# Optimization experiments

Measured on AMD Instinct MI355X. Metric: run time of the kernel, lower is better.

Reference implementation:

```python
import jax, jax.numpy as jnp
import numpy as np

N_FIELDS = 8
HIDDEN = 128
GEO = 15
APP = 32
N_PTS = 524288


def setup_inputs() -> dict:
    key = jax.random.key(0)
    ks = jax.random.split(key, 12)
    cin = 3 + GEO + APP  # color-net input dim = 50
    s = 0.05
    return {
        "positions": jax.random.normal(ks[0], (N_PTS, 3), jnp.float32),
        "directions": jax.random.normal(ks[1], (N_PTS, 3), jnp.float32),
        "appearance_embedding": jax.random.normal(ks[2], (N_PTS, APP), jnp.float32),
        "centroids": jax.random.normal(ks[3], (N_FIELDS, 3), jnp.float32),
        "Wd1": jax.random.normal(ks[4], (N_FIELDS, 3, HIDDEN), jnp.float32) * s,
        "bd1": jnp.zeros((N_FIELDS, HIDDEN), jnp.float32),
        "Wd2": jax.random.normal(ks[5], (N_FIELDS, HIDDEN, 1 + GEO), jnp.float32) * s,
        "bd2": jnp.zeros((N_FIELDS, 1 + GEO), jnp.float32),
        "Wc1": jax.random.normal(ks[6], (N_FIELDS, cin, HIDDEN), jnp.float32) * s,
        "bc1": jnp.zeros((N_FIELDS, HIDDEN), jnp.float32),
        "Wc2": jax.random.normal(ks[7], (N_FIELDS, HIDDEN, 3), jnp.float32) * s,
        "bc2": jnp.zeros((N_FIELDS, 3), jnp.float32),
    }


def reference(positions, directions, appearance_embedding, centroids,
              Wd1, bd1, Wd2, bd2, Wc1, bc1, Wc2, bc2):
    # --- routing: nearest centroid (cdist + argmin); squared dist has same argmin ---
    d2 = jnp.sum((positions[:, None, :] - centroids[None, :, :]) ** 2, axis=-1)  # [N, F]
    assign = jnp.argmin(d2, axis=1)  # [N] int

    n = positions.shape[0]
    density = jnp.zeros((n, 1), positions.dtype)
    rgb = jnp.zeros((n, 3), positions.dtype)

    # dispatch/combine: masked dense evaluation per field (small fixed field count)
    for i in range(N_FIELDS):
        mask = (assign == i)[:, None]
        # field.density_fn: 2-layer MLP, trunc_exp density activation
        h = jax.nn.relu(positions @ Wd1[i] + bd1[i])          # [N, H]
        dout = h @ Wd2[i] + bd2[i]                            # [N, 1+GEO]
        dens_i = jnp.exp(dout[:, :1])                         # trunc_exp
        geo_i = dout[:, 1:]                                   # density embedding
        # field.get_outputs: color head on (dirs, geo_feat, appearance)
        cin = jnp.concatenate([directions, geo_i, appearance_embedding], axis=-1)
        hc = jax.nn.relu(cin @ Wc1[i] + bc1[i])               # [N, H]
        rgb_i = jax.nn.sigmoid(hc @ Wc2[i] + bc2[i])          # [N, 3]
        density = jnp.where(mask, dens_i, density)
        rgb = jnp.where(mask, rgb_i, rgb)

    # outputs concatenated: [density | rgb] -> [N, 4]
    return jnp.concatenate([density, rgb], axis=-1)
```

## Files before the change

kernel.cpp:

```cpp
#include <hip/hip_runtime.h>
#include <math.h>

#define NF 8
#define HID 128
#define TILE 576
#define NIT 9

typedef _Float16 f16;
typedef _Float16 h2 __attribute__((ext_vector_type(2)));
typedef _Float16 f16x8 __attribute__((ext_vector_type(8)));
typedef float f32x4 __attribute__((ext_vector_type(4)));
typedef unsigned int u32;
typedef u32 u32x2 __attribute__((ext_vector_type(2)));
typedef u32 u32x4 __attribute__((ext_vector_type(4)));

__device__ __forceinline__ u32 pk(float a, float b) {
    return __builtin_bit_cast(u32, __builtin_amdgcn_cvt_pkrtz(a, b));
}
__device__ __forceinline__ float dot2a(u32 a, u32 b, float c) {
    return __builtin_amdgcn_fdot2(__builtin_bit_cast(h2, a),
                                  __builtin_bit_cast(h2, b), c, false);
}


__device__ __forceinline__ int assign_field(float px, float py, float pz,
                                            const float* __restrict__ cen) {
    int best = 0;
    float bd = 3.4e38f;
#pragma unroll
    for (int k = 0; k < NF; ++k) {
        float dx = px - cen[k * 3 + 0];
        float dy = py - cen[k * 3 + 1];
        float dz = pz - cen[k * 3 + 2];
        float d = fmaf(dx, dx, fmaf(dy, dy, dz * dz));
        if (d < bd) { bd = d; best = k; }
    }
    return best;
}

__global__ void k_count(const float* __restrict__ pos, const float* __restrict__ cen,
                        int n, int* __restrict__ blockcnt) {
    __shared__ int lc[NF];
    int tid = threadIdx.x;
    if (tid < NF) lc[tid] = 0;
    __syncthreads();
    int i4 = blockIdx.x * blockDim.x + tid;
    int base = i4 * 4;
    if (base + 3 < n) {
        const float4* p4 = (const float4*)pos;
        float4 a = p4[i4 * 3 + 0];
        float4 b = p4[i4 * 3 + 1];
        float4 c = p4[i4 * 3 + 2];
        atomicAdd(&lc[assign_field(a.x, a.y, a.z, cen)], 1);
        atomicAdd(&lc[assign_field(a.w, b.x, b.y, cen)], 1);
        atomicAdd(&lc[assign_field(b.z, b.w, c.x, cen)], 1);
        atomicAdd(&lc[assign_field(c.y, c.z, c.w, cen)], 1);
    } else {
        for (int i = base; i < n; ++i)
            atomicAdd(&lc[assign_field(pos[3 * i], pos[3 * i + 1], pos[3 * i + 2], cen)], 1);
    }
    __syncthreads();
    if (tid < NF) blockcnt[blockIdx.x * NF + tid] = lc[tid];
}

__global__ void k_scatscan(const float* __restrict__ pos, const float* __restrict__ cen,
                           int n, int nb, int* __restrict__ ws) {
    const int tid = threadIdx.x;
    const int f = tid >> 6, lane = tid & 63;
    const int* c = ws + 32;
    int* perm = ws + 32 + nb * NF;
    __shared__ int totals[NF], pres[NF], starts[NF], cur[NF];

    int tot = 0, pre = 0;
    for (int b = lane; b < nb; b += 64) {
        int v = c[b * NF + f];
        tot += v;
        if (b < (int)blockIdx.x) pre += v;
    }
#pragma unroll
    for (int d = 1; d < 64; d <<= 1) {
        tot += __shfl_xor(tot, d, 64);
        pre += __shfl_xor(pre, d, 64);
    }
    if (lane == 0) { totals[f] = tot; pres[f] = pre; }
    __syncthreads();
    if (tid == 0) {
        int s = 0, tp = 0;
        for (int k = 0; k < NF; ++k) {
            starts[k] = s;
            if (blockIdx.x == 0) {
                ws[k] = totals[k];
                ws[8 + k] = s;
                ws[16 + k] = tp;
            }
            s += totals[k];
            tp += (totals[k] + TILE - 1) / TILE;
        }
        if (blockIdx.x == 0) ws[24] = tp;
    }
    __syncthreads();
    if (tid < NF) cur[tid] = starts[tid] + pres[tid];
    __syncthreads();

    int i4 = blockIdx.x * blockDim.x + tid;
    int base = i4 * 4;
    if (base + 3 < n) {
        const float4* p4 = (const float4*)pos;
        float4 a = p4[i4 * 3 + 0];
        float4 b = p4[i4 * 3 + 1];
        float4 cc = p4[i4 * 3 + 2];
        int f0 = assign_field(a.x, a.y, a.z, cen);
        int f1 = assign_field(a.w, b.x, b.y, cen);
        int f2 = assign_field(b.z, b.w, cc.x, cen);
        int f3 = assign_field(cc.y, cc.z, cc.w, cen);
        perm[atomicAdd(&cur[f0], 1)] = base;
        perm[atomicAdd(&cur[f1], 1)] = base + 1;
        perm[atomicAdd(&cur[f2], 1)] = base + 2;
        perm[atomicAdd(&cur[f3], 1)] = base + 3;
    } else {
        for (int i = base; i < n; ++i) {
            int ff = assign_field(pos[3 * i], pos[3 * i + 1], pos[3 * i + 2], cen);
            perm[atomicAdd(&cur[ff], 1)] = i;
        }
    }
}

__global__ __launch_bounds__(256, 3) void k_main(
    const float* __restrict__ positions, const float* __restrict__ directions,
    const float* __restrict__ app,
    const float* __restrict__ Wd1, const float* __restrict__ bd1,
    const float* __restrict__ Wd2, const float* __restrict__ bd2,
    const float* __restrict__ Wc1, const float* __restrict__ bc1,
    const float* __restrict__ Wc2, const float* __restrict__ bc2,
    const int* __restrict__ ws, int nb, float* __restrict__ out) {
    const int b = blockIdx.x;
    if (b >= ws[24]) return;
    int f = 0;
#pragma unroll
    for (int k = 1; k < NF; ++k) if (b >= ws[16 + k]) f = k;
    const int tile = b - ws[16 + f];
    const int cnt = ws[f];
    const int start = ws[8 + f];
    const int* perm = ws + 32 + nb * NF;
    const int tid = threadIdx.x;
    const int w = tid >> 6, lane = tid & 63;
    const int pt = lane & 15, quad = lane >> 4;

    __shared__ __align__(16) f16 sWc1t[HID * 72];
    __shared__ __align__(16) u32 sWc2p[64 * 4];
    __shared__ __align__(16) int sIdx[4][16];
    __shared__ __align__(16) u32x2 sDir[4][16];
    __shared__ __align__(16) f16 sGeo[4][16][16];
    __shared__ __align__(16) f16 sH[4][16 * 136];

    if (tid < HID) {
        int h = tid;
        f16* row = &sWc1t[h * 72];
        const float* Wf = Wc1 + f * 50 * HID;
        row[0] = (f16)Wf[0 * HID + h];
        row[1] = (f16)Wf[1 * HID + h];
        row[2] = (f16)Wf[2 * HID + h];
        row[3] = (f16)bc1[f * HID + h];
        row[4] = 0; row[5] = 0; row[6] = 0; row[7] = 0;
        for (int a = 0; a < 32; ++a) row[8 + a] = (f16)Wf[(18 + a) * HID + h];
        for (int g = 0; g < 15; ++g) row[40 + g] = (f16)Wf[(3 + g) * HID + h];
        for (int z = 55; z < 72; ++z) row[z] = 0;
    }
    if (tid >= 128 && tid < 192) {
        int hp = tid - 128;
        const float* W2 = Wc2 + f * HID * 3;
        sWc2p[hp * 4 + 0] = pk(W2[(2 * hp) * 3 + 0], W2[(2 * hp + 1) * 3 + 0]);
        sWc2p[hp * 4 + 1] = pk(W2[(2 * hp) * 3 + 1], W2[(2 * hp + 1) * 3 + 1]);
        sWc2p[hp * 4 + 2] = pk(W2[(2 * hp) * 3 + 2], W2[(2 * hp + 1) * 3 + 2]);
        sWc2p[hp * 4 + 3] = 0;
    }
    if (lane < 16) sGeo[w][pt][15] = (f16)0.f;

    u32 wd1a0[8], wd1a1[8];
    if (quad == 0) {
        const float* W1 = Wd1 + f * 3 * HID;
        const float* B1 = bd1 + f * HID;
#pragma unroll
        for (int mt = 0; mt < 8; ++mt) {
            int m = 16 * mt + pt;
            wd1a0[mt] = pk(W1[m], W1[HID + m]);
            wd1a1[mt] = pk(W1[2 * HID + m], B1[m]);
        }
    } else {
#pragma unroll
        for (int mt = 0; mt < 8; ++mt) { wd1a0[mt] = 0; wd1a1[mt] = 0; }
    }
    f16x8 wd2b[4];
    {
        const float* W2d = Wd2 + f * HID * 16;
#pragma unroll
        for (int s = 0; s < 4; ++s) {
            u32x4 v;
#pragma unroll
            for (int jp = 0; jp < 4; ++jp) {
                int k = quad * 8 + 32 * s + 2 * jp;
                v[jp] = pk(W2d[k * 16 + pt], W2d[(k + 1) * 16 + pt]);
            }
            wd2b[s] = __builtin_bit_cast(f16x8, v);
        }
    }
    const float bd2v = bd2[f * 16 + pt];
    const float c20 = bc2[f * 3 + 0], c21 = bc2[f * 3 + 1], c22 = bc2[f * 3 + 2];
    __syncthreads();

    const int tstart = tile * TILE;
    const int cidx = (quad == 0) ? 3 : (quad - 1);

    int g_idx;
    float4 g_c0, g_c1;
    float g_p0, g_p1, g_p2;
    {
        int plc = tstart + w * 16 + pt;
        if (plc > cnt - 1) plc = cnt - 1;
        g_idx = perm[start + plc];
        const float4* ap = (const float4*)(app + g_idx * 32 + cidx * 8);
        g_c0 = ap[0]; g_c1 = ap[1];
        if (quad == 0) {
            g_p0 = positions[g_idx * 3 + 0];
            g_p1 = positions[g_idx * 3 + 1];
            g_p2 = positions[g_idx * 3 + 2];
        } else if (quad == 1) {
            g_p0 = directions[g_idx * 3 + 0];
            g_p1 = directions[g_idx * 3 + 1];
            g_p2 = directions[g_idx * 3 + 2];
        }
    }

#pragma unroll 1
    for (int it = 0; it < NIT; ++it) {
        const int pbase = tstart + it * 64 + w * 16;
        if (pbase >= cnt) break;

        const int cur_idx = g_idx;
        const float4 cur_c0 = g_c0, cur_c1 = g_c1;
        const float cp0 = g_p0, cp1 = g_p1, cp2 = g_p2;
        if (quad == 0) {
            sIdx[w][pt] = cur_idx;
        } else if (quad == 1) {
            u32x2 d2; d2.x = pk(cp0, cp1); d2.y = pk(cp2, 1.f);
            sDir[w][pt] = d2;
        }

        {
            const int nbase = tstart + (it + 1) * 64 + w * 16;
            if (it + 1 < NIT && nbase < cnt) {
                int plc = nbase + pt;
                if (plc > cnt - 1) plc = cnt - 1;
                g_idx = perm[start + plc];
                const float4* ap = (const float4*)(app + g_idx * 32 + cidx * 8);
                g_c0 = ap[0]; g_c1 = ap[1];
                if (quad == 0) {
                    g_p0 = positions[g_idx * 3 + 0];
                    g_p1 = positions[g_idx * 3 + 1];
                    g_p2 = positions[g_idx * 3 + 2];
                } else if (quad == 1) {
                    g_p0 = directions[g_idx * 3 + 0];
                    g_p1 = directions[g_idx * 3 + 1];
                    g_p2 = directions[g_idx * 3 + 2];
                }
            }
        }

        __builtin_amdgcn_s_setprio(1);

        u32x4 xv;
        xv.x = (quad == 0) ? pk(cp0, cp1) : 0u;
        xv.y = (quad == 0) ? pk(cp2, 1.f) : 0u;
        xv.z = 0u; xv.w = 0u;
        const f16x8 xb = __builtin_bit_cast(f16x8, xv);
#pragma unroll
        for (int mt = 0; mt < 8; ++mt) {
            u32x4 av; av.x = wd1a0[mt]; av.y = wd1a1[mt]; av.z = 0u; av.w = 0u;
            f16x8 af = __builtin_bit_cast(f16x8, av);
            f32x4 acc = {0.f, 0.f, 0.f, 0.f};
            acc = __builtin_amdgcn_mfma_f32_16x16x32_f16(af, xb, acc, 0, 0, 0);
            u32x2 hw;
            hw.x = pk(fmaxf(acc[0], 0.f), fmaxf(acc[1], 0.f));
            hw.y = pk(fmaxf(acc[2], 0.f), fmaxf(acc[3], 0.f));
            *(u32x2*)&sH[w][pt * 136 + 16 * mt + quad * 4] = hw;
        }

        f32x4 dacc = {bd2v, bd2v, bd2v, bd2v};
#pragma unroll
        for (int s = 0; s < 4; ++s) {
            f16x8 ha = __builtin_bit_cast(f16x8,
                *(const u32x4*)&sH[w][pt * 136 + quad * 8 + 32 * s]);
            dacc = __builtin_amdgcn_mfma_f32_16x16x32_f16(ha, wd2b[s], dacc, 0, 0, 0);
        }
        if (pt == 0) {
            int4 si = *(const int4*)&sIdx[w][quad * 4];
            out[si.x * 4] = __expf(dacc[0]);
            out[si.y * 4] = __expf(dacc[1]);
            out[si.z * 4] = __expf(dacc[2]);
            out[si.w * 4] = __expf(dacc[3]);
        } else {
#pragma unroll
            for (int r = 0; r < 4; ++r)
                sGeo[w][quad * 4 + r][pt - 1] = (f16)dacc[r];
        }

        u32x4 capp;
        capp.x = pk(cur_c0.x, cur_c0.y); capp.y = pk(cur_c0.z, cur_c0.w);
        capp.z = pk(cur_c1.x, cur_c1.y); capp.w = pk(cur_c1.z, cur_c1.w);
        f16x8 cb0, cb1;
        {
            u32x4 t0 = capp;
            if (quad == 0) {
                u32x2 d2 = sDir[w][pt];
                t0.x = d2.x; t0.y = d2.y; t0.z = 0u; t0.w = 0u;
            }
            cb0 = __builtin_bit_cast(f16x8, t0);
            u32x4 t1;
            if (quad == 0) t1 = capp;
            else if (quad == 3) { t1.x = 0u; t1.y = 0u; t1.z = 0u; t1.w = 0u; }
            else t1 = *(const u32x4*)&sGeo[w][pt][(quad - 1) * 8];
            cb1 = __builtin_bit_cast(f16x8, t1);
        }
        float r0 = 0.f, r1 = 0.f, r2 = 0.f;
#pragma unroll
        for (int mt = 0; mt < 8; ++mt) {
            f16x8 wa0 = __builtin_bit_cast(f16x8,
                *(const u32x4*)&sWc1t[(16 * mt + pt) * 72 + quad * 8]);
            f16x8 wa1 = __builtin_bit_cast(f16x8,
                *(const u32x4*)&sWc1t[(16 * mt + pt) * 72 + quad * 8 + 32]);
            f32x4 cacc = {0.f, 0.f, 0.f, 0.f};
            cacc = __builtin_amdgcn_mfma_f32_16x16x32_f16(wa0, cb0, cacc, 0, 0, 0);
            cacc = __builtin_amdgcn_mfma_f32_16x16x32_f16(wa1, cb1, cacc, 0, 0, 0);
            u32 h01 = pk(fmaxf(cacc[0], 0.f), fmaxf(cacc[1], 0.f));
            u32 h23 = pk(fmaxf(cacc[2], 0.f), fmaxf(cacc[3], 0.f));
            u32x4 w01 = *(const u32x4*)&sWc2p[(8 * mt + 2 * quad) * 4];
            u32x4 w23 = *(const u32x4*)&sWc2p[(8 * mt + 2 * quad + 1) * 4];
            r0 = dot2a(h01, w01.x, r0); r0 = dot2a(h23, w23.x, r0);
            r1 = dot2a(h01, w01.y, r1); r1 = dot2a(h23, w23.y, r1);
            r2 = dot2a(h01, w01.z, r2); r2 = dot2a(h23, w23.z, r2);
        }
        __builtin_amdgcn_s_setprio(0);

        r0 += __shfl_xor(r0, 16, 64); r0 += __shfl_xor(r0, 32, 64);
        r1 += __shfl_xor(r1, 16, 64); r1 += __shfl_xor(r1, 32, 64);
        r2 += __shfl_xor(r2, 16, 64); r2 += __shfl_xor(r2, 32, 64);
        if (quad == 0) {
            float s0 = 1.f / (1.f + __expf(-(r0 + c20)));
            float s1 = 1.f / (1.f + __expf(-(r1 + c21)));
            float s2 = 1.f / (1.f + __expf(-(r2 + c22)));
            out[cur_idx * 4 + 1] = s0;
            *(float2*)&out[cur_idx * 4 + 2] = make_float2(s1, s2);
        }
    }
}

extern "C" void kernel_launch(void* const* d_in, const int* in_sizes, int n_in,
                              void* d_out, int out_size, void* d_ws, size_t ws_size,
                              hipStream_t stream) {
    const float* positions = (const float*)d_in[0];
    const float* directions = (const float*)d_in[1];
    const float* app = (const float*)d_in[2];
    const float* centroids = (const float*)d_in[3];
    const float* Wd1 = (const float*)d_in[4];
    const float* bd1 = (const float*)d_in[5];
    const float* Wd2 = (const float*)d_in[6];
    const float* bd2 = (const float*)d_in[7];
    const float* Wc1 = (const float*)d_in[8];
    const float* bc1 = (const float*)d_in[9];
    const float* Wc2 = (const float*)d_in[10];
    const float* bc2 = (const float*)d_in[11];
    float* out = (float*)d_out;
    int* wsi = (int*)d_ws;
    const int n = in_sizes[0] / 3;
    const int nb = (n + 2047) / 2048;
    const int max_tiles = (n + TILE - 1) / TILE + NF;

    k_count<<<nb, 512, 0, stream>>>(positions, centroids, n, wsi + 32);
    k_scatscan<<<nb, 512, 0, stream>>>(positions, centroids, n, nb, wsi);
    k_main<<<max_tiles, 256, 0, stream>>>(positions, directions, app, Wd1, bd1, Wd2,
                                          bd2, Wc1, bc1, Wc2, bc2, wsi, nb, out);
}
```

Baseline: 58.49 us.

## Merge count and scatter passes into one kernel using global atomic bucket offsets

Replaces the two-pass count-then-scan-scatter routing with a single prep kernel. Each block counts its points per field in shared memory, reserves a range in a per-field global bucket of size n with one atomic add per field, then writes its permutation entries. The main kernel now computes field tile offsets itself from the totals. This removes one kernel launch and the second read of positions, at the cost of a memset, global atomics, a workspace of 8·n entries and a non-deterministic point order within each field.

```diff
diff --git a/kernel.cpp b/kernel.cpp
--- a/kernel.cpp
+++ b/kernel.cpp
@@ -38,90 +38,47 @@
     return best;
 }
 
-__global__ void k_count(const float* __restrict__ pos, const float* __restrict__ cen,
-                        int n, int* __restrict__ blockcnt) {
-    __shared__ int lc[NF];
-    int tid = threadIdx.x;
+__global__ void k_prep(const float* __restrict__ pos, const float* __restrict__ cen,
+                       int n, int* __restrict__ ws) {
+    __shared__ int lc[NF], lbase[NF];
+    int* perm = ws + 32;
+    const int tid = threadIdx.x;
     if (tid < NF) lc[tid] = 0;
     __syncthreads();
+
     int i4 = blockIdx.x * blockDim.x + tid;
     int base = i4 * 4;
-    if (base + 3 < n) {
+    int fj[4], rj[4];
+    int m = n - base;
+    if (m < 0) m = 0;
+    if (m > 4) m = 4;
+    if (m == 4) {
         const float4* p4 = (const float4*)pos;
         float4 a = p4[i4 * 3 + 0];
         float4 b = p4[i4 * 3 + 1];
         float4 c = p4[i4 * 3 + 2];
-        atomicAdd(&lc[assign_field(a.x, a.y, a.z, cen)], 1);
-        atomicAdd(&lc[assign_field(a.w, b.x, b.y, cen)], 1);
-        atomicAdd(&lc[assign_field(b.z, b.w, c.x, cen)], 1);
-        atomicAdd(&lc[assign_field(c.y, c.z, c.w, cen)], 1);
+        fj[0] = assign_field(a.x, a.y, a.z, cen);
+        fj[1] = assign_field(a.w, b.x, b.y, cen);
+        fj[2] = assign_field(b.z, b.w, c.x, cen);
+        fj[3] = assign_field(c.y, c.z, c.w, cen);
+#pragma unroll
+        for (int j = 0; j < 4; ++j) rj[j] = atomicAdd(&lc[fj[j]], 1);
     } else {
-        for (int i = base; i < n; ++i)
-            atomicAdd(&lc[assign_field(pos[3 * i], pos[3 * i + 1], pos[3 * i + 2], cen)], 1);
+#pragma unroll
+        for (int j = 0; j < 4; ++j) {
+            if (j < m) {
+                int i = base + j;
+                fj[j] = assign_field(pos[3 * i], pos[3 * i + 1], pos[3 * i + 2], cen);
+                rj[j] = atomicAdd(&lc[fj[j]], 1);
+            }
+        }
     }
     __syncthreads();
-    if (tid < NF) blockcnt[blockIdx.x * NF + tid] = lc[tid];
-}
-
-__global__ void k_scatscan(const float* __restrict__ pos, const float* __restrict__ cen,
-                           int n, int nb, int* __restrict__ ws) {
-    const int tid = threadIdx.x;
-    const int f = tid >> 6, lane = tid & 63;
-    const int* c = ws + 32;
-    int* perm = ws + 32 + nb * NF;
-    __shared__ int totals[NF], pres[NF], starts[NF], cur[NF];
-
-    int tot = 0, pre = 0;
-    for (int b = lane; b < nb; b += 64) {
-        int v = c[b * NF + f];
-        tot += v;
-        if (b < (int)blockIdx.x) pre += v;
-    }
-#pragma unroll
-    for (int d = 1; d < 64; d <<= 1) {
-        tot += __shfl_xor(tot, d, 64);
-        pre += __shfl_xor(pre, d, 64);
-    }
-    if (lane == 0) { totals[f] = tot; pres[f] = pre; }
+    if (tid < NF) lbase[tid] = atomicAdd(&ws[tid], lc[tid]);
     __syncthreads();
-    if (tid == 0) {
-        int s = 0, tp = 0;
-        for (int k = 0; k < NF; ++k) {
-            starts[k] = s;
-            if (blockIdx.x == 0) {
-                ws[k] = totals[k];
-                ws[8 + k] = s;
-                ws[16 + k] = tp;
-            }
-            s += totals[k];
-            tp += (totals[k] + TILE - 1) / TILE;
-        }
-        if (blockIdx.x == 0) ws[24] = tp;
-    }
-    __syncthreads();
-    if (tid < NF) cur[tid] = starts[tid] + pres[tid];
-    __syncthreads();
-
-    int i4 = blockIdx.x * blockDim.x + tid;
-    int base = i4 * 4;
-    if (base + 3 < n) {
-        const float4* p4 = (const float4*)pos;
-        float4 a = p4[i4 * 3 + 0];
-        float4 b = p4[i4 * 3 + 1];
-        float4 cc = p4[i4 * 3 + 2];
-        int f0 = assign_field(a.x, a.y, a.z, cen);
-        int f1 = assign_field(a.w, b.x, b.y, cen);
-        int f2 = assign_field(b.z, b.w, cc.x, cen);
-        int f3 = assign_field(cc.y, cc.z, cc.w, cen);
-        perm[atomicAdd(&cur[f0], 1)] = base;
-        perm[atomicAdd(&cur[f1], 1)] = base + 1;
-        perm[atomicAdd(&cur[f2], 1)] = base + 2;
-        perm[atomicAdd(&cur[f3], 1)] = base + 3;
-    } else {
-        for (int i = base; i < n; ++i) {
-            int ff = assign_field(pos[3 * i], pos[3 * i + 1], pos[3 * i + 2], cen);
-            perm[atomicAdd(&cur[ff], 1)] = i;
-        }
+#pragma unroll
+    for (int j = 0; j < 4; ++j) {
+        if (j < m) perm[fj[j] * n + lbase[fj[j]] + rj[j]] = base + j;
     }
 }
 
@@ -132,16 +89,19 @@
     const float* __restrict__ Wd2, const float* __restrict__ bd2,
     const float* __restrict__ Wc1, const float* __restrict__ bc1,
     const float* __restrict__ Wc2, const float* __restrict__ bc2,
-    const int* __restrict__ ws, int nb, float* __restrict__ out) {
+    const int* __restrict__ ws, int n, float* __restrict__ out) {
     const int b = blockIdx.x;
-    if (b >= ws[24]) return;
-    int f = 0;
-#pragma unroll
-    for (int k = 1; k < NF; ++k) if (b >= ws[16 + k]) f = k;
-    const int tile = b - ws[16 + f];
-    const int cnt = ws[f];
-    const int start = ws[8 + f];
-    const int* perm = ws + 32 + nb * NF;
+    int f = -1, tile = 0, acc = 0, cnt = 0;
+#pragma unroll
+    for (int k = 0; k < NF; ++k) {
+        int ck = ws[k];
+        int tk = (ck + TILE - 1) / TILE;
+        if (f < 0 && b < acc + tk) { f = k; tile = b - acc; cnt = ck; }
+        acc += tk;
+    }
+    if (f < 0) return;
+    const int start = f * n;
+    const int* perm = ws + 32;
     const int tid = threadIdx.x;
     const int w = tid >> 6, lane = tid & 63;
     const int pt = lane & 15, quad = lane >> 4;
@@ -375,8 +335,8 @@
     const int nb = (n + 2047) / 2048;
     const int max_tiles = (n + TILE - 1) / TILE + NF;
 
-    k_count<<<nb, 512, 0, stream>>>(positions, centroids, n, wsi + 32);
-    k_scatscan<<<nb, 512, 0, stream>>>(positions, centroids, n, nb, wsi);
+    hipMemsetAsync(d_ws, 0, 32, stream);
+    k_prep<<<nb, 512, 0, stream>>>(positions, centroids, n, wsi);
     k_main<<<max_tiles, 256, 0, stream>>>(positions, directions, app, Wd1, bd1, Wd2,
-                                          bd2, Wc1, bc1, Wc2, bc2, wsi, nb, out);
-}
+                                          bd2, Wc1, bc1, Wc2, bc2, wsi, n, out);
+}
```

Result: slower. 59.75 us (+2.1%).
